# Kernel tuning notes

Hardware: AMD Instinct MI355X
Metric: run time of the kernel (lower is better)

The kernel has to match this reference:

```python
import jax, jax.numpy as jnp
import numpy as np
from jax import lax

EPS = 1e-6
RADIUS = (5, 5, 5)          # box-filter window (must be odd for shape consistency)
GRADIENT_TYPE = "symmetric"  # {'active','passive','symmetric'}
SHAPE = (1, 1, 256, 256, 256)


def _box1d(x, axis, k):
    """Running-sum (integral image) 1D box filter of width k, 'same' padding floor(k/2)."""
    pad = (k - 1) // 2
    cfg = [(0, 0)] * x.ndim
    cfg[axis] = (pad, pad)
    xp = jnp.pad(x, cfg)
    c = jnp.cumsum(xp, axis=axis)
    cfg2 = [(0, 0)] * x.ndim
    cfg2[axis] = (1, 0)
    c = jnp.pad(c, cfg2)
    n = c.shape[axis]
    return lax.slice_in_dim(c, k, n, axis=axis) - lax.slice_in_dim(c, 0, n - k, axis=axis)


def _box3d(x):
    # separable uniform (all-ones) 3D box filter == F.conv3d with ones kernel
    for ax, k in zip((2, 3, 4), RADIUS):
        x = _box1d(x, ax, k)
    return x


def _grad1d(x, axis):
    """torch.gradient: central differences inside, one-sided at the edges, spacing=1."""
    n = x.shape[axis]
    central = (lax.slice_in_dim(x, 2, n, axis=axis) - lax.slice_in_dim(x, 0, n - 2, axis=axis)) * 0.5
    first = lax.slice_in_dim(x, 1, 2, axis=axis) - lax.slice_in_dim(x, 0, 1, axis=axis)
    last = lax.slice_in_dim(x, n - 1, n, axis=axis) - lax.slice_in_dim(x, n - 2, n - 1, axis=axis)
    return jnp.concatenate([first, central, last], axis=axis)


def _ncc_forces(image, reference_image):
    npix = float(np.prod(RADIUS))
    sum_i = _box3d(image)
    sum_r = _box3d(reference_image)
    sum_ii = _box3d(image * image)
    sum_rr = _box3d(reference_image * reference_image)
    sum_ir = _box3d(image * reference_image)

    image_mean = sum_i / npix
    reference_image_mean = sum_i / npix  # NOTE: faithful to original (uses sum_i, not sum_r)

    var_r = sum_rr - 2.0 * reference_image_mean * sum_r + npix * reference_image_mean * reference_image_mean
    var_i = sum_ii - 2.0 * image_mean * sum_i + npix * image_mean * image_mean
    cross = (sum_ir - reference_image_mean * sum_i - image_mean * sum_r
             + npix * image_mean * reference_image_mean)

    if GRADIENT_TYPE == "active":
        grads = [_grad1d(image, a) for a in (2, 3, 4)]
    elif GRADIENT_TYPE == "passive":
        grads = [_grad1d(reference_image, a) for a in (2, 3, 4)]
    elif GRADIENT_TYPE == "symmetric":
        grads = [0.5 * (_grad1d(image, a) + _grad1d(reference_image, a)) for a in (2, 3, 4)]
    else:
        raise ValueError("Unknown gradient type")

    factor = 2.0 * cross / (var_i * var_r + EPS) * (image - cross / var_r * reference_image)
    return -factor * jnp.concatenate(grads, axis=1)  # (B, 3, D, H, W)


def setup_inputs() -> dict:
    key = jax.random.key(0)
    k1, k2 = jax.random.split(key)
    return {
        "image": jax.random.normal(k1, SHAPE, dtype=jnp.float32),
        "mask": jnp.ones(SHAPE, dtype=jnp.float32),
        "reference_image": jax.random.normal(k2, SHAPE, dtype=jnp.float32),
        "reference_mask": jnp.ones(SHAPE, dtype=jnp.float32),
    }


def reference(image, mask, reference_image, reference_mask):
    # mask / reference_mask are accepted but unused, exactly as in the original module.
    return _ncc_forces(image, reference_image)
```

## Files before the change

kernel.cpp:

```cpp
#include <hip/hip_runtime.h>


#define DIM 256
#define TX  32
#define TY  8
#define ZCH 64
#define PXA 40
#define PY  12
#define NT  256
#define RS  5

__global__ __launch_bounds__(NT, 4) void ncc_forces_kernel(
    const float* __restrict__ gI,
    const float* __restrict__ gR,
    float* __restrict__ gOut)
{
    __shared__ __align__(16) float rawI[RS][PY][PXA];
    __shared__ __align__(16) float rawR[RS][PY][PXA];
    __shared__ float ytmp[5][TY][PXA];

    const int t  = threadIdx.x;
    const int tx = t & 31;
    const int ty = t >> 5;
    const int x0 = blockIdx.x * TX;
    const int y0 = blockIdx.y * TY;
    const int z0 = blockIdx.z * ZCH;

    const bool pfI   = (t < 120);
    const bool pfR   = (t >= 128 && t < 248);
    const bool pfAct = pfI || pfR;
    const int  pid   = pfI ? t : (t - 128);
    const int  prow  = pid / 10;
    const int  pcol  = (pid - prow * 10) * 4;
    const int  pgy   = y0 - 2 + prow;
    const int  pgx   = x0 - 4 + pcol;
    const float* pbase = pfI ? gI : gR;
    float*       praw  = pfI ? &rawI[0][0][0] : &rawR[0][0][0];
    const bool   pxyOk = ((unsigned)pgy < DIM) && ((unsigned)pgx < DIM);

    const bool bAct = (t < 160);
    const int  brow = t / 20;
    const int  bcol = (t - brow * 20) * 2;

    float4 pf = make_float4(0.f, 0.f, 0.f, 0.f);

    if (pfAct) {
        float4 v = make_float4(0.f, 0.f, 0.f, 0.f);
        const int zp0 = z0 - 2;
        if (zp0 >= 0 && pxyOk)
            v = *(const float4*)(pbase + (((size_t)zp0 * DIM + pgy) * DIM + pgx));
        *(float4*)(praw + (((z0 - 2 + 10) % RS) * PY + prow) * PXA + pcol) = v;
        const int zp1 = z0 - 1;
        if (zp1 >= 0 && pxyOk)
            pf = *(const float4*)(pbase + (((size_t)zp1 * DIM + pgy) * DIM + pgx));
    }

    float h[4][5];
    #pragma unroll
    for (int j = 0; j < 4; ++j)
        #pragma unroll
        for (int f = 0; f < 5; ++f) h[j][f] = 0.f;

    __syncthreads();

    for (int z = z0 - 2; z < z0 + ZCH + 2; ++z) {
        const int sz  = (z + 10) % RS;
        const int szn = (z + 11) % RS;

        if (pfAct) {
            *(float4*)(praw + (szn * PY + prow) * PXA + pcol) = pf;
            float4 v = make_float4(0.f, 0.f, 0.f, 0.f);
            const int zp = z + 2;
            if (zp < DIM && pxyOk)
                v = *(const float4*)(pbase + (((size_t)zp * DIM + pgy) * DIM + pgx));
            pf = v;
        }

        if (bAct) {
            float sA0=0.f,sA1=0.f,sB0=0.f,sB1=0.f,sAA0=0.f,sAA1=0.f,
                  sBB0=0.f,sBB1=0.f,sAB0=0.f,sAB1=0.f;
            #pragma unroll
            for (int dy = 0; dy < 5; ++dy) {
                const float aI0 = rawI[sz][brow + dy][bcol];
                const float aI1 = rawI[sz][brow + dy][bcol + 1];
                const float aR0 = rawR[sz][brow + dy][bcol];
                const float aR1 = rawR[sz][brow + dy][bcol + 1];
                sA0 += aI0; sA1 += aI1; sB0 += aR0; sB1 += aR1;
                sAA0 = fmaf(aI0, aI0, sAA0); sAA1 = fmaf(aI1, aI1, sAA1);
                sBB0 = fmaf(aR0, aR0, sBB0); sBB1 = fmaf(aR1, aR1, sBB1);
                sAB0 = fmaf(aI0, aR0, sAB0); sAB1 = fmaf(aI1, aR1, sAB1);
            }
            ytmp[0][brow][bcol] = sA0;  ytmp[0][brow][bcol + 1] = sA1;
            ytmp[1][brow][bcol] = sB0;  ytmp[1][brow][bcol + 1] = sB1;
            ytmp[2][brow][bcol] = sAA0; ytmp[2][brow][bcol + 1] = sAA1;
            ytmp[3][brow][bcol] = sBB0; ytmp[3][brow][bcol + 1] = sBB1;
            ytmp[4][brow][bcol] = sAB0; ytmp[4][brow][bcol + 1] = sAB1;
        }
        __syncthreads();

        float n[5];
        #pragma unroll
        for (int f = 0; f < 5; ++f) {
            const float* yp = &ytmp[f][ty][tx];
            n[f] = yp[2] + yp[3] + yp[4] + yp[5] + yp[6];
        }

        const int zc = z - 2;
        if (zc >= z0) {
            float zs[5];
            #pragma unroll
            for (int f = 0; f < 5; ++f)
                zs[f] = h[0][f] + h[1][f] + h[2][f] + h[3][f] + n[f];

            const float m     = zs[0] * (1.0f / 125.0f);
            const float var_r = zs[3] - 2.0f * m * zs[1] + 125.0f * m * m;
            const float var_i = zs[2] - 2.0f * m * zs[0] + 125.0f * m * m;
            const float cross = zs[4] - m * zs[0] - m * zs[1] + 125.0f * m * m;

            const int sc = (zc + 10) % RS;
            const int sm = (zc + 9)  % RS;
            const int sp = (zc + 11) % RS;
            const int ly = ty + 2, lx = tx + 4;

            const float ic = rawI[sc][ly][lx];
            const float rc = rawR[sc][ly][lx];

            float giz, grz;
            if (zc == 0) {
                giz = rawI[sp][ly][lx] - ic;
                grz = rawR[sp][ly][lx] - rc;
            } else if (zc == DIM - 1) {
                giz = ic - rawI[sm][ly][lx];
                grz = rc - rawR[sm][ly][lx];
            } else {
                giz = 0.5f * (rawI[sp][ly][lx] - rawI[sm][ly][lx]);
                grz = 0.5f * (rawR[sp][ly][lx] - rawR[sm][ly][lx]);
            }

            const int gy = y0 + ty;
            float giy, gry;
            if (gy == 0) {
                giy = rawI[sc][ly + 1][lx] - ic;
                gry = rawR[sc][ly + 1][lx] - rc;
            } else if (gy == DIM - 1) {
                giy = ic - rawI[sc][ly - 1][lx];
                gry = rc - rawR[sc][ly - 1][lx];
            } else {
                giy = 0.5f * (rawI[sc][ly + 1][lx] - rawI[sc][ly - 1][lx]);
                gry = 0.5f * (rawR[sc][ly + 1][lx] - rawR[sc][ly - 1][lx]);
            }

            const int gx = x0 + tx;
            float gix, grx;
            if (gx == 0) {
                gix = rawI[sc][ly][lx + 1] - ic;
                grx = rawR[sc][ly][lx + 1] - rc;
            } else if (gx == DIM - 1) {
                gix = ic - rawI[sc][ly][lx - 1];
                grx = rc - rawR[sc][ly][lx - 1];
            } else {
                gix = 0.5f * (rawI[sc][ly][lx + 1] - rawI[sc][ly][lx - 1]);
                grx = 0.5f * (rawR[sc][ly][lx + 1] - rawR[sc][ly][lx - 1]);
            }

            const float inv_d = __builtin_amdgcn_rcpf(fmaf(var_i, var_r, 1e-6f));
            const float inv_r = __builtin_amdgcn_rcpf(var_r);
            const float factor = 2.0f * cross * inv_d * (ic - cross * inv_r * rc);

            const size_t CS   = (size_t)DIM * DIM * DIM;
            const size_t base = ((size_t)zc * DIM + gy) * DIM + gx;
            gOut[base]          = -factor * 0.5f * (giz + grz);
            gOut[base + CS]     = -factor * 0.5f * (giy + gry);
            gOut[base + 2 * CS] = -factor * 0.5f * (gix + grx);
        }

        #pragma unroll
        for (int f = 0; f < 5; ++f) {
            h[0][f] = h[1][f]; h[1][f] = h[2][f]; h[2][f] = h[3][f]; h[3][f] = n[f];
        }
        __syncthreads();
    }
}

extern "C" void kernel_launch(void* const* d_in, const int* in_sizes, int n_in,
                              void* d_out, int out_size, void* d_ws, size_t ws_size,
                              hipStream_t stream) {
    const float* img = (const float*)d_in[0];
    const float* ref = (const float*)d_in[2];
    float* out = (float*)d_out;

    dim3 grid(DIM / TX, DIM / TY, DIM / ZCH);
    ncc_forces_kernel<<<grid, NT, 0, stream>>>(img, ref, out);
}
```

Before: 399.8 us.

## Shrink z-ring to 4 slots, interleave y-sum layout, keep z-center values in registers

The raw-plane ring buffer drops from 5 to 4 slots, so slot indexing becomes a bitmask instead of a modulo. The y-direction partial sums are stored interleaved per column (5 fields plus padding) so each thread reads them with float2 loads, and only the 36 columns actually needed are computed. Centre I/R values are kept in a register history, so the z-gradient no longer reads neighbouring planes from shared memory. The z-chunk is halved to 32 for more blocks, at the cost of more halo reloads, and the occupancy hint in launch_bounds is removed.

```diff
diff --git a/kernel.cpp b/kernel.cpp
--- a/kernel.cpp
+++ b/kernel.cpp
@@ -4,20 +4,22 @@
 #define DIM 256
 #define TX  32
 #define TY  8
-#define ZCH 64
+#define ZCH 32
 #define PXA 40
 #define PY  12
+#define YJ  36
 #define NT  256
-#define RS  5
-
-__global__ __launch_bounds__(NT, 4) void ncc_forces_kernel(
+#define RS  4
+#define SLOT(p) (((p) + 4) & 3)
+
+__global__ __launch_bounds__(NT) void ncc_forces_kernel(
     const float* __restrict__ gI,
     const float* __restrict__ gR,
     float* __restrict__ gOut)
 {
     __shared__ __align__(16) float rawI[RS][PY][PXA];
     __shared__ __align__(16) float rawR[RS][PY][PXA];
-    __shared__ float ytmp[5][TY][PXA];
+    __shared__ __align__(16) float ytmp[TY][YJ][6];
 
     const int t  = threadIdx.x;
     const int tx = t & 31;
@@ -38,9 +40,9 @@
     float*       praw  = pfI ? &rawI[0][0][0] : &rawR[0][0][0];
     const bool   pxyOk = ((unsigned)pgy < DIM) && ((unsigned)pgx < DIM);
 
-    const bool bAct = (t < 160);
-    const int  brow = t / 20;
-    const int  bcol = (t - brow * 20) * 2;
+    const bool bAct = (t < 144);
+    const int  brow = t / 18;
+    const int  bj   = (t - brow * 18) * 2;
 
     float4 pf = make_float4(0.f, 0.f, 0.f, 0.f);
 
@@ -49,7 +51,7 @@
         const int zp0 = z0 - 2;
         if (zp0 >= 0 && pxyOk)
             v = *(const float4*)(pbase + (((size_t)zp0 * DIM + pgy) * DIM + pgx));
-        *(float4*)(praw + (((z0 - 2 + 10) % RS) * PY + prow) * PXA + pcol) = v;
+        *(float4*)(praw + (SLOT(z0 - 2) * PY + prow) * PXA + pcol) = v;
         const int zp1 = z0 - 1;
         if (zp1 >= 0 && pxyOk)
             pf = *(const float4*)(pbase + (((size_t)zp1 * DIM + pgy) * DIM + pgx));
@@ -61,11 +63,14 @@
         #pragma unroll
         for (int f = 0; f < 5; ++f) h[j][f] = 0.f;
 
+    float hI0 = 0.f, hI1 = 0.f, hI2 = 0.f, hI3 = 0.f;
+    float hR0 = 0.f, hR1 = 0.f, hR2 = 0.f, hR3 = 0.f;
+
     __syncthreads();
 
     for (int z = z0 - 2; z < z0 + ZCH + 2; ++z) {
-        const int sz  = (z + 10) % RS;
-        const int szn = (z + 11) % RS;
+        const int sz  = SLOT(z);
+        const int szn = SLOT(z + 1);
 
         if (pfAct) {
             *(float4*)(praw + (szn * PY + prow) * PXA + pcol) = pf;
@@ -76,91 +81,99 @@
             pf = v;
         }
 
+        {
+            const float cI = rawI[sz][ty + 2][tx + 4];
+            const float cR = rawR[sz][ty + 2][tx + 4];
+            hI0 = hI1; hI1 = hI2; hI2 = hI3; hI3 = cI;
+            hR0 = hR1; hR1 = hR2; hR2 = hR3; hR3 = cR;
+        }
+
         if (bAct) {
-            float sA0=0.f,sA1=0.f,sB0=0.f,sB1=0.f,sAA0=0.f,sAA1=0.f,
-                  sBB0=0.f,sBB1=0.f,sAB0=0.f,sAB1=0.f;
+            float2 sA  = make_float2(0.f, 0.f), sB  = make_float2(0.f, 0.f);
+            float2 sAA = make_float2(0.f, 0.f), sBB = make_float2(0.f, 0.f);
+            float2 sAB = make_float2(0.f, 0.f);
             #pragma unroll
             for (int dy = 0; dy < 5; ++dy) {
-                const float aI0 = rawI[sz][brow + dy][bcol];
-                const float aI1 = rawI[sz][brow + dy][bcol + 1];
-                const float aR0 = rawR[sz][brow + dy][bcol];
-                const float aR1 = rawR[sz][brow + dy][bcol + 1];
-                sA0 += aI0; sA1 += aI1; sB0 += aR0; sB1 += aR1;
-                sAA0 = fmaf(aI0, aI0, sAA0); sAA1 = fmaf(aI1, aI1, sAA1);
-                sBB0 = fmaf(aR0, aR0, sBB0); sBB1 = fmaf(aR1, aR1, sBB1);
-                sAB0 = fmaf(aI0, aR0, sAB0); sAB1 = fmaf(aI1, aR1, sAB1);
-            }
-            ytmp[0][brow][bcol] = sA0;  ytmp[0][brow][bcol + 1] = sA1;
-            ytmp[1][brow][bcol] = sB0;  ytmp[1][brow][bcol + 1] = sB1;
-            ytmp[2][brow][bcol] = sAA0; ytmp[2][brow][bcol + 1] = sAA1;
-            ytmp[3][brow][bcol] = sBB0; ytmp[3][brow][bcol + 1] = sBB1;
-            ytmp[4][brow][bcol] = sAB0; ytmp[4][brow][bcol + 1] = sAB1;
+                const float2 aI = *(const float2*)&rawI[sz][brow + dy][bj + 2];
+                const float2 aR = *(const float2*)&rawR[sz][brow + dy][bj + 2];
+                sA.x += aI.x;  sA.y += aI.y;
+                sB.x += aR.x;  sB.y += aR.y;
+                sAA.x = fmaf(aI.x, aI.x, sAA.x); sAA.y = fmaf(aI.y, aI.y, sAA.y);
+                sBB.x = fmaf(aR.x, aR.x, sBB.x); sBB.y = fmaf(aR.y, aR.y, sBB.y);
+                sAB.x = fmaf(aI.x, aR.x, sAB.x); sAB.y = fmaf(aI.y, aR.y, sAB.y);
+            }
+            float* y0p = &ytmp[brow][bj][0];
+            float* y1p = &ytmp[brow][bj + 1][0];
+            *(float2*)(y0p)     = make_float2(sA.x,  sB.x);
+            *(float2*)(y0p + 2) = make_float2(sAA.x, sBB.x);
+            *(float2*)(y0p + 4) = make_float2(sAB.x, 0.f);
+            *(float2*)(y1p)     = make_float2(sA.y,  sB.y);
+            *(float2*)(y1p + 2) = make_float2(sAA.y, sBB.y);
+            *(float2*)(y1p + 4) = make_float2(sAB.y, 0.f);
         }
         __syncthreads();
 
-        float n[5];
+        float n0 = 0.f, n1 = 0.f, n2 = 0.f, n3 = 0.f, n4 = 0.f;
         #pragma unroll
-        for (int f = 0; f < 5; ++f) {
-            const float* yp = &ytmp[f][ty][tx];
-            n[f] = yp[2] + yp[3] + yp[4] + yp[5] + yp[6];
+        for (int k = 0; k < 5; ++k) {
+            const float* yp = &ytmp[ty][tx + k][0];
+            const float2 p01 = *(const float2*)yp;
+            const float2 p23 = *(const float2*)(yp + 2);
+            n0 += p01.x; n1 += p01.y; n2 += p23.x; n3 += p23.y; n4 += yp[4];
         }
 
         const int zc = z - 2;
         if (zc >= z0) {
-            float zs[5];
-            #pragma unroll
-            for (int f = 0; f < 5; ++f)
-                zs[f] = h[0][f] + h[1][f] + h[2][f] + h[3][f] + n[f];
-
-            const float m     = zs[0] * (1.0f / 125.0f);
-            const float var_r = zs[3] - 2.0f * m * zs[1] + 125.0f * m * m;
-            const float var_i = zs[2] - 2.0f * m * zs[0] + 125.0f * m * m;
-            const float cross = zs[4] - m * zs[0] - m * zs[1] + 125.0f * m * m;
-
-            const int sc = (zc + 10) % RS;
-            const int sm = (zc + 9)  % RS;
-            const int sp = (zc + 11) % RS;
-            const int ly = ty + 2, lx = tx + 4;
-
-            const float ic = rawI[sc][ly][lx];
-            const float rc = rawR[sc][ly][lx];
+            const float zs0 = h[0][0] + h[1][0] + h[2][0] + h[3][0] + n0;
+            const float zs1 = h[0][1] + h[1][1] + h[2][1] + h[3][1] + n1;
+            const float zs2 = h[0][2] + h[1][2] + h[2][2] + h[3][2] + n2;
+            const float zs3 = h[0][3] + h[1][3] + h[2][3] + h[3][3] + n3;
+            const float zs4 = h[0][4] + h[1][4] + h[2][4] + h[3][4] + n4;
+
+            const float m     = zs0 * (1.0f / 125.0f);
+            const float var_r = zs3 - 2.0f * m * zs1 + 125.0f * m * m;
+            const float var_i = zs2 - 2.0f * m * zs0 + 125.0f * m * m;
+            const float cross = zs4 - m * zs0 - m * zs1 + 125.0f * m * m;
+
+            const float ic = hI1;
+            const float rc = hR1;
 
             float giz, grz;
             if (zc == 0) {
-                giz = rawI[sp][ly][lx] - ic;
-                grz = rawR[sp][ly][lx] - rc;
+                giz = hI2 - ic;  grz = hR2 - rc;
             } else if (zc == DIM - 1) {
-                giz = ic - rawI[sm][ly][lx];
-                grz = rc - rawR[sm][ly][lx];
+                giz = ic - hI0;  grz = rc - hR0;
             } else {
-                giz = 0.5f * (rawI[sp][ly][lx] - rawI[sm][ly][lx]);
-                grz = 0.5f * (rawR[sp][ly][lx] - rawR[sm][ly][lx]);
-            }
+                giz = 0.5f * (hI2 - hI0);  grz = 0.5f * (hR2 - hR0);
+            }
+
+            const int szc = SLOT(zc);
+            const int ly  = ty + 2, lx = tx + 4;
 
             const int gy = y0 + ty;
             float giy, gry;
             if (gy == 0) {
-                giy = rawI[sc][ly + 1][lx] - ic;
-                gry = rawR[sc][ly + 1][lx] - rc;
+                giy = rawI[szc][ly + 1][lx] - ic;
+                gry = rawR[szc][ly + 1][lx] - rc;
             } else if (gy == DIM - 1) {
-                giy = ic - rawI[sc][ly - 1][lx];
-                gry = rc - rawR[sc][ly - 1][lx];
+                giy = ic - rawI[szc][ly - 1][lx];
+                gry = rc - rawR[szc][ly - 1][lx];
             } else {
-                giy = 0.5f * (rawI[sc][ly + 1][lx] - rawI[sc][ly - 1][lx]);
-                gry = 0.5f * (rawR[sc][ly + 1][lx] - rawR[sc][ly - 1][lx]);
+                giy = 0.5f * (rawI[szc][ly + 1][lx] - rawI[szc][ly - 1][lx]);
+                gry = 0.5f * (rawR[szc][ly + 1][lx] - rawR[szc][ly - 1][lx]);
             }
 
             const int gx = x0 + tx;
             float gix, grx;
             if (gx == 0) {
-                gix = rawI[sc][ly][lx + 1] - ic;
-                grx = rawR[sc][ly][lx + 1] - rc;
+                gix = rawI[szc][ly][lx + 1] - ic;
+                grx = rawR[szc][ly][lx + 1] - rc;
             } else if (gx == DIM - 1) {
-                gix = ic - rawI[sc][ly][lx - 1];
-                grx = rc - rawR[sc][ly][lx - 1];
+                gix = ic - rawI[szc][ly][lx - 1];
+                grx = rc - rawR[szc][ly][lx - 1];
             } else {
-                gix = 0.5f * (rawI[sc][ly][lx + 1] - rawI[sc][ly][lx - 1]);
-                grx = 0.5f * (rawR[sc][ly][lx + 1] - rawR[sc][ly][lx - 1]);
+                gix = 0.5f * (rawI[szc][ly][lx + 1] - rawI[szc][ly][lx - 1]);
+                grx = 0.5f * (rawR[szc][ly][lx + 1] - rawR[szc][ly][lx - 1]);
             }
 
             const float inv_d = __builtin_amdgcn_rcpf(fmaf(var_i, var_r, 1e-6f));
@@ -176,8 +189,10 @@
 
         #pragma unroll
         for (int f = 0; f < 5; ++f) {
-            h[0][f] = h[1][f]; h[1][f] = h[2][f]; h[2][f] = h[3][f]; h[3][f] = n[f];
-        }
+            h[0][f] = h[1][f]; h[1][f] = h[2][f]; h[2][f] = h[3][f];
+        }
+        h[3][0] = n0; h[3][1] = n1; h[3][2] = n2; h[3][3] = n3; h[3][4] = n4;
+
         __syncthreads();
     }
 }
```

Result: slower. 413.1 us (+3.3%).
